# Kernel tuning notes

Measured on AMD Instinct MI355X. Metric: run time of the kernel, lower is better.

Reference implementation:

```python
import jax, jax.numpy as jnp
import numpy as np

N_NODES = 8192
SEQ = 256
H = 32  # lstm_hdim == gcn_hdim


def lstm_layer(x, Wih, Whh, bih, bhh, return_seq):
    # x: [B, S, D] -> torch nn.LSTM, gate order i,f,g,o
    B = x.shape[0]
    Hd = Whh.shape[1]
    b = bih + bhh

    def step(carry, xt):
        h, c = carry
        z = xt @ Wih.T + h @ Whh.T + b  # [B, 4H]
        i, f, g, o = jnp.split(z, 4, axis=-1)
        c = jax.nn.sigmoid(f) * c + jax.nn.sigmoid(i) * jnp.tanh(g)
        h = jax.nn.sigmoid(o) * jnp.tanh(c)
        return (h, c), (h if return_seq else None)

    init = (jnp.zeros((B, Hd), x.dtype), jnp.zeros((B, Hd), x.dtype))
    (h_n, _), ys = jax.lax.scan(step, init, jnp.transpose(x, (1, 0, 2)))
    if return_seq:
        ys = jnp.transpose(ys, (1, 0, 2))  # [B, S, H]
    return ys, h_n


def layer_norm(x, g, b, eps=1e-5):
    mu = jnp.mean(x, axis=-1, keepdims=True)
    var = jnp.mean((x - mu) ** 2, axis=-1, keepdims=True)
    return (x - mu) * jax.lax.rsqrt(var + eps) * g + b


def gcn_conv(x, edge_index, edge_weight, W, bias, n_nodes):
    # PyG GCNConv with self-loops (fill 1.0) and symmetric normalization.
    h = x @ W  # transform first (in_dim -> out_dim)
    src, dst = edge_index[0], edge_index[1]
    deg = jax.ops.segment_sum(edge_weight, dst, num_segments=n_nodes) + 1.0  # +1 self loop
    dinv = jnp.where(deg > 0, jax.lax.rsqrt(deg), 0.0)
    norm = dinv[src] * edge_weight * dinv[dst]  # [E]
    agg = jax.ops.segment_sum(norm[:, None] * h[src], dst, num_segments=n_nodes)
    agg = agg + h * (dinv * dinv)[:, None]  # self-loop message
    return agg + bias


def setup_inputs() -> dict:
    key = jax.random.key(0)
    ks = jax.random.split(key, 20)
    s = 0.1
    d = {
        "x": jax.random.normal(ks[0], (N_NODES, SEQ), jnp.float32),
        "edge_weight": jax.random.uniform(ks[1], (262144,), jnp.float32),
        "Wih1": jax.random.normal(ks[2], (4 * H, 1)) * s,
        "Whh1": jax.random.normal(ks[3], (4 * H, H)) * s,
        "bih1": jax.random.normal(ks[4], (4 * H,)) * s,
        "bhh1": jax.random.normal(ks[5], (4 * H,)) * s,
        "ln1_g": jnp.ones((H,), jnp.float32),
        "ln1_b": jnp.zeros((H,), jnp.float32),
        "Wih2": jax.random.normal(ks[6], (4 * H, H)) * s,
        "Whh2": jax.random.normal(ks[7], (4 * H, H)) * s,
        "bih2": jax.random.normal(ks[8], (4 * H,)) * s,
        "bhh2": jax.random.normal(ks[9], (4 * H,)) * s,
        "Wg1": jax.random.normal(ks[10], (H, H)) * s,
        "bg1": jax.random.normal(ks[11], (H,)) * s,
        "Wg2": jax.random.normal(ks[12], (H, H)) * s,
        "bg2": jax.random.normal(ks[13], (H,)) * s,
        "Wfc": jax.random.normal(ks[14], (2, H + 1)) * s,
        "bfc": jax.random.normal(ks[15], (2,)) * s,
        "edge_index": jax.random.randint(ks[16], (2, 262144), 0, N_NODES, jnp.int64 if jax.config.jax_enable_x64 else jnp.int32),
    }
    return d


def reference(x, edge_weight, Wih1, Whh1, bih1, bhh1, ln1_g, ln1_b,
              Wih2, Whh2, bih2, bhh2, Wg1, bg1, Wg2, bg2, Wfc, bfc, edge_index):
    n = x.shape[0]
    xs = x[:, :, None]  # [B, S, 1]
    # Temporal module (batched over all samples; dropout off in eval).
    y1, _ = lstm_layer(xs, Wih1, Whh1, bih1, bhh1, return_seq=True)
    y1 = layer_norm(y1, ln1_g, ln1_b)
    _, h2 = lstm_layer(y1, Wih2, Whh2, bih2, bhh2, return_seq=False)  # [B, H]
    gcn_in = h2  # lstm_out.view(-1, lstm_hdim)
    # Spatial module: 2 GCNConv + ELU (dropout between layers is identity in eval).
    g = jax.nn.elu(gcn_conv(gcn_in, edge_index, edge_weight, Wg1, bg1, n))
    g = jax.nn.elu(gcn_conv(g, edge_index, edge_weight, Wg2, bg2, n))
    feat = jnp.concatenate([gcn_in, jnp.mean(g, axis=1, keepdims=True)], axis=1)  # [B, H+1]
    out = feat @ Wfc.T + bfc
    return jax.nn.log_softmax(out, axis=1)
```

## Files before the change

kernel.cpp:

```cpp
#include <hip/hip_runtime.h>

typedef __attribute__((ext_vector_type(8))) short short8;
typedef __attribute__((ext_vector_type(4))) float float4v;

#define NNODES 8192
#define SEQLEN 256

static __device__ __forceinline__ float bf2f(unsigned short u) {
  union { unsigned u; float f; } v; v.u = ((unsigned)u) << 16; return v.f;
}
static __device__ __forceinline__ unsigned short f2bf(float f) {
  union { float f; unsigned u; } v; v.f = f;
  unsigned r = v.u + 0x7FFFu + ((v.u >> 16) & 1u);
  return (unsigned short)(r >> 16);
}
static __device__ __forceinline__ void splitbf8(const float* v, short8& hi) {
#pragma unroll
  for (int j = 0; j < 8; ++j) hi[j] = (short)f2bf(v[j]);
}

static __device__ __forceinline__ float lstm_cell(float zi, float zf, float zg,
                                                  float zo, float& c) {
  float ef = __builtin_amdgcn_exp2f(-zf);
  float ei = __builtin_amdgcn_exp2f(-zi);
  float eg = __builtin_amdgcn_exp2f(fminf(zg + zg, 60.f));
  float fterm = c * __builtin_amdgcn_rcpf(1.f + ef);
  float igt = (eg - 1.f) * __builtin_amdgcn_rcpf((1.f + ei) * (eg + 1.f));
  c = fterm + igt;
  float eo = __builtin_amdgcn_exp2f(-zo);
  float ec = __builtin_amdgcn_exp2f(fminf(2.88539008178f * c, 40.f));
  return (ec - 1.f) * __builtin_amdgcn_rcpf((1.f + eo) * (ec + 1.f));
}

__global__ __launch_bounds__(512, 4)
void lstm_fused(const float* __restrict__ x,
                const float* __restrict__ Wih1, const float* __restrict__ Whh1,
                const float* __restrict__ bih1, const float* __restrict__ bhh1,
                const float* __restrict__ ln_g, const float* __restrict__ ln_b,
                const float* __restrict__ Wih2, const float* __restrict__ Whh2,
                const float* __restrict__ bih2, const float* __restrict__ bhh2,
                const float* __restrict__ Wg1,
                float* __restrict__ h2out, float* __restrict__ hWa)
{
  const int tid = threadIdx.x;
  const int w = tid >> 6;
  const int lane = tid & 63;
  const int c = lane & 15;
  const int q = lane >> 4;
  const int cn = lane >> 2;
  const int ch = lane & 3;
  const int hid = w * 4 + ch;
  const int nodeBase = blockIdx.x * 16;
  const float L = 1.44269504089f;

  __shared__ __align__(16) float xlds[16 * 260];
  __shared__ __align__(16) float zbuf1[16 * 132];
  __shared__ __align__(16) float zbuf2[16 * 132];
  __shared__ __align__(16) unsigned short h1p[2][16 * 40];
  __shared__ __align__(16) unsigned short h2p[2][16 * 40];
  __shared__ __align__(16) float mu2[32];
  __shared__ __align__(16) float wgbuf[32 * 33];
  __shared__ __align__(16) float h2f[16 * 33];

  for (int i = tid; i < 16 * 256; i += 512) {
    int nn = i >> 8, tt = i & 255;
    xlds[nn * 260 + tt] = x[(size_t)(nodeBase + nn) * SEQLEN + tt];
  }
  if (tid < 64) xlds[(tid >> 2) * 260 + 256 + (tid & 3)] = 0.f;
  for (int i = tid; i < 1024; i += 512) wgbuf[(i >> 5) * 33 + (i & 31)] = Wg1[i];

  const int brow = (c & 3) * 32 + w * 4 + (c >> 2);
  short8 Bh1, Bi2, Bh2;
  float Gpre, b1pre, b2pre;
  {
    float v[8];
#pragma unroll
    for (int j = 0; j < 8; ++j) v[j] = L * Whh1[brow * 32 + q * 8 + j];
    splitbf8(v, Bh1);
#pragma unroll
    for (int j = 0; j < 8; ++j) v[j] = L * Wih2[brow * 32 + q * 8 + j] * ln_g[q * 8 + j];
    splitbf8(v, Bi2);
#pragma unroll
    for (int j = 0; j < 8; ++j) v[j] = L * Whh2[brow * 32 + q * 8 + j];
    splitbf8(v, Bh2);
    float sG = 0.f, sB = 0.f;
    for (int k = 0; k < 32; ++k) {
      sG += Wih2[brow * 32 + k] * ln_g[k];
      sB += Wih2[brow * 32 + k] * ln_b[k];
    }
    Gpre = L * sG;
    b1pre = L * (bih1[brow] + bhh1[brow]);
    b2pre = L * (sB + bih2[brow] + bhh2[brow]);
  }
  const float4v C1 = {b1pre, b1pre, b1pre, b1pre};
  const float4v C2 = {b2pre, b2pre, b2pre, b2pre};
  const float4v z4 = {0.f, 0.f, 0.f, 0.f};
  float w1v[4];
#pragma unroll
  for (int g = 0; g < 4; ++g) w1v[g] = L * Wih1[g * 32 + hid];

  int zW[4];
#pragma unroll
  for (int r = 0; r < 4; ++r) zW[r] = (q * 4 + r) * 132 + w * 16 + c;
  const int zR = cn * 132 + hid * 4;
  const int hWr = cn * 40 + hid;
  const int hRd = c * 40 + q * 8;

  short8 h1A = {0,0,0,0,0,0,0,0};
  short8 h2A = {0,0,0,0,0,0,0,0};
  float c1 = 0.f, c2 = 0.f, hv2 = 0.f;
  __syncthreads();

  {
    float4v za = __builtin_amdgcn_mfma_f32_16x16x32_bf16(h1A, Bh1, C1, 0, 0, 0);
#pragma unroll
    for (int r = 0; r < 4; ++r) zbuf1[zW[r]] = za[r];
    float4v zv = *(const float4v*)&zbuf1[zR];
    float xv = xlds[cn * 260 + 0];
    float hv = lstm_cell(fmaf(xv, w1v[0], zv[0]), fmaf(xv, w1v[1], zv[1]),
                         fmaf(xv, w1v[2], zv[2]), fmaf(xv, w1v[3], zv[3]), c1);
    h1p[1][hWr] = f2bf(hv);
  }
  __syncthreads();
  h1A = *(const short8*)&h1p[1][hRd];

  for (int t = 0; t < SEQLEN; ++t) {
    const int pl = t & 1;
    float4v za = __builtin_amdgcn_mfma_f32_16x16x32_bf16(h1A, Bh1, C1, 0, 0, 0);
    float4v db = __builtin_amdgcn_mfma_f32_16x16x32_bf16(h2A, Bh2, C2, 0, 0, 0);

    float s = 0.f, s2 = 0.f;
#pragma unroll
    for (int j = 0; j < 8; ++j) {
      float hf = bf2f((unsigned short)h1A[j]);
      s += hf; s2 = fmaf(hf, hf, s2);
    }
    s  += __shfl_xor(s, 16, 64);  s  += __shfl_xor(s, 32, 64);
    s2 += __shfl_xor(s2, 16, 64); s2 += __shfl_xor(s2, 32, 64);
    float mu = s * (1.f / 32.f);
    float var = s2 * (1.f / 32.f) - mu * mu;
    float rstd = rsqrtf(var + 1e-5f);
    if (q < 2) mu2[c * 2 + q] = (q == 0) ? rstd : rstd * mu;

    float4v da = __builtin_amdgcn_mfma_f32_16x16x32_bf16(h1A, Bi2, z4, 0, 0, 0);
#pragma unroll
    for (int r = 0; r < 4; ++r) {
      float2 ab = *(const float2*)&mu2[(q * 4 + r) * 2];
      zbuf2[zW[r]] = fmaf(ab.x, da[r], fmaf(-ab.y, Gpre, db[r]));
      zbuf1[zW[r]] = za[r];
    }
    {
      float4v zv = *(const float4v*)&zbuf2[zR];
      hv2 = lstm_cell(zv[0], zv[1], zv[2], zv[3], c2);
      h2p[pl][hWr] = f2bf(hv2);
    }
    {
      float4v zv = *(const float4v*)&zbuf1[zR];
      float xv = xlds[cn * 260 + t + 1];
      float hv = lstm_cell(fmaf(xv, w1v[0], zv[0]), fmaf(xv, w1v[1], zv[1]),
                           fmaf(xv, w1v[2], zv[2]), fmaf(xv, w1v[3], zv[3]), c1);
      h1p[pl][hWr] = f2bf(hv);
    }
    __syncthreads();
    h1A = *(const short8*)&h1p[pl][hRd];
    h2A = *(const short8*)&h2p[pl][hRd];
  }

  h2out[(size_t)(nodeBase + cn) * 32 + hid] = hv2;

  __syncthreads();
  h2f[cn * 33 + hid] = hv2;
  __syncthreads();
  {
    int nl = tid >> 5, j = tid & 31;
    float acc = 0.f;
#pragma unroll
    for (int k = 0; k < 32; ++k) acc = fmaf(h2f[nl * 33 + k], wgbuf[k * 33 + j], acc);
    hWa[(size_t)(nodeBase + nl) * 32 + j] = acc;
  }
}

__global__ void count_k(const int* __restrict__ ei, const float* __restrict__ ew,
                        unsigned long long* __restrict__ pk, int E) {
  int e = blockIdx.x * 256 + threadIdx.x;
  if (e >= E) return;
  int d = ei[E + e];
  unsigned long long pay = (1ull << 40) |
      (unsigned long long)(unsigned)(ew[e] * 16777216.f + 0.5f);
  atomicAdd(&pk[d], pay);
}

__global__ __launch_bounds__(1024, 1)
void scan_k(const unsigned long long* __restrict__ pk, int* __restrict__ off,
            int* __restrict__ pos, float* __restrict__ dinv) {
  __shared__ int wtot[16];
  __shared__ int wexcl[16];
  int tid = threadIdx.x;
  int wv = tid >> 6, lane = tid & 63;
  int base = tid * 8;
  int v[8]; int sum = 0;
#pragma unroll
  for (int i = 0; i < 8; ++i) {
    unsigned long long u = pk[base + i];
    v[i] = (int)(u >> 40);
    float degv = (float)(u & 0xFFFFFFFFFFull) * (1.f / 16777216.f);
    dinv[base + i] = rsqrtf(degv + 1.0f);
    sum += v[i];
  }
  int incl = sum;
#pragma unroll
  for (int d = 1; d < 64; d <<= 1) {
    int t = __shfl_up(incl, d, 64);
    if (lane >= d) incl += t;
  }
  if (lane == 63) wtot[wv] = incl;
  __syncthreads();
  if (wv == 0 && lane < 16) {
    int wval = wtot[lane];
    int wincl = wval;
#pragma unroll
    for (int d = 1; d < 16; d <<= 1) {
      int t = __shfl_up(wincl, d, 64);
      if (lane >= d) wincl += t;
    }
    wexcl[lane] = wincl - wval;
  }
  __syncthreads();
  int run = wexcl[wv] + (incl - sum);
#pragma unroll
  for (int i = 0; i < 8; ++i) {
    off[base + i] = run; pos[base + i] = run; run += v[i];
  }
  if (tid == 1023) off[8192] = run;
}

__global__ void scatter_k(const int* __restrict__ ei, const float* __restrict__ ew,
                          const float* __restrict__ dinv, int* __restrict__ pos,
                          int2* __restrict__ ed, int E) {
  int e = blockIdx.x * 256 + threadIdx.x;
  if (e >= E) return;
  int sidx = ei[e], d = ei[E + e];
  int p = atomicAdd(&pos[d], 1);
  int2 pay;
  pay.x = sidx;
  pay.y = __float_as_int(dinv[sidx] * ew[e] * dinv[d]);
  ed[p] = pay;
}

__global__ __launch_bounds__(512, 4)
void gather_mid_k(const int* __restrict__ off, const int2* __restrict__ ed,
                  const float* __restrict__ dinv, const float* __restrict__ hWa,
                  const float* __restrict__ bg1, const float* __restrict__ Wg2,
                  float* __restrict__ aggB) {
  __shared__ float wg[32 * 33];
  __shared__ float g1buf[16][33];
  int tid = threadIdx.x;
  for (int i = tid; i < 1024; i += 512) wg[(i >> 5) * 33 + (i & 31)] = Wg2[i];
  int nl = tid >> 5, j = tid & 31;
  int node = blockIdx.x * 16 + nl;
  float dv = dinv[node];
  float a0 = dv * dv * hWa[(size_t)node * 32 + j];
  float a1 = 0.f, a2 = 0.f, a3 = 0.f;
  int p0 = off[node], p1 = off[node + 1];
  int p = p0;
  for (; p + 3 < p1; p += 4) {
    int2 e0 = ed[p], e1 = ed[p + 1], e2 = ed[p + 2], e3 = ed[p + 3];
    a0 = fmaf(__int_as_float(e0.y), hWa[(size_t)e0.x * 32 + j], a0);
    a1 = fmaf(__int_as_float(e1.y), hWa[(size_t)e1.x * 32 + j], a1);
    a2 = fmaf(__int_as_float(e2.y), hWa[(size_t)e2.x * 32 + j], a2);
    a3 = fmaf(__int_as_float(e3.y), hWa[(size_t)e3.x * 32 + j], a3);
  }
  for (; p < p1; ++p) {
    int2 e0 = ed[p];
    a0 = fmaf(__int_as_float(e0.y), hWa[(size_t)e0.x * 32 + j], a0);
  }
  float v = (a0 + a1) + (a2 + a3) + bg1[j];
  g1buf[nl][j] = (v > 0.f) ? v : expm1f(v);
  __syncthreads();
  float acc = 0.f;
#pragma unroll
  for (int k = 0; k < 32; ++k) acc = fmaf(g1buf[nl][k], wg[k * 33 + j], acc);
  aggB[(size_t)node * 32 + j] = acc;
}

__global__ __launch_bounds__(512, 4)
void gather_final_k(const int* __restrict__ off, const int2* __restrict__ ed,
                    const float* __restrict__ dinv, const float* __restrict__ aggB,
                    const float* __restrict__ bg2, const float* __restrict__ h2o,
                    const float* __restrict__ Wfc, const float* __restrict__ bfc,
                    float* __restrict__ out) {
  int tid = threadIdx.x;
  int nl = tid >> 5, j = tid & 31;
  int node = blockIdx.x * 16 + nl;
  float dv = dinv[node];
  float a0 = dv * dv * aggB[(size_t)node * 32 + j];
  float a1 = 0.f, a2 = 0.f, a3 = 0.f;
  int p0 = off[node], p1 = off[node + 1];
  int p = p0;
  for (; p + 3 < p1; p += 4) {
    int2 e0 = ed[p], e1 = ed[p + 1], e2 = ed[p + 2], e3 = ed[p + 3];
    a0 = fmaf(__int_as_float(e0.y), aggB[(size_t)e0.x * 32 + j], a0);
    a1 = fmaf(__int_as_float(e1.y), aggB[(size_t)e1.x * 32 + j], a1);
    a2 = fmaf(__int_as_float(e2.y), aggB[(size_t)e2.x * 32 + j], a2);
    a3 = fmaf(__int_as_float(e3.y), aggB[(size_t)e3.x * 32 + j], a3);
  }
  for (; p < p1; ++p) {
    int2 e0 = ed[p];
    a0 = fmaf(__int_as_float(e0.y), aggB[(size_t)e0.x * 32 + j], a0);
  }
  float v = (a0 + a1) + (a2 + a3) + bg2[j];
  float e = (v > 0.f) ? v : expm1f(v);
  float h2v = h2o[(size_t)node * 32 + j];
  float p0s = h2v * Wfc[j];
  float p1s = h2v * Wfc[33 + j];
#pragma unroll
  for (int m = 1; m < 32; m <<= 1) {
    e   += __shfl_xor(e, m, 32);
    p0s += __shfl_xor(p0s, m, 32);
    p1s += __shfl_xor(p1s, m, 32);
  }
  if (j == 0) {
    float mean = e * (1.f / 32.f);
    float o0 = p0s + mean * Wfc[32] + bfc[0];
    float o1 = p1s + mean * Wfc[65] + bfc[1];
    float mx = fmaxf(o0, o1);
    float l = mx + logf(expf(o0 - mx) + expf(o1 - mx));
    out[node * 2 + 0] = o0 - l;
    out[node * 2 + 1] = o1 - l;
  }
}

extern "C" void kernel_launch(void* const* d_in, const int* in_sizes, int n_in,
                              void* d_out, int out_size, void* d_ws, size_t ws_size,
                              hipStream_t stream) {
  const float* x    = (const float*)d_in[0];
  const float* ew   = (const float*)d_in[1];
  const float* Wih1 = (const float*)d_in[2];
  const float* Whh1 = (const float*)d_in[3];
  const float* bih1 = (const float*)d_in[4];
  const float* bhh1 = (const float*)d_in[5];
  const float* ln_g = (const float*)d_in[6];
  const float* ln_b = (const float*)d_in[7];
  const float* Wih2 = (const float*)d_in[8];
  const float* Whh2 = (const float*)d_in[9];
  const float* bih2 = (const float*)d_in[10];
  const float* bhh2 = (const float*)d_in[11];
  const float* Wg1  = (const float*)d_in[12];
  const float* bg1  = (const float*)d_in[13];
  const float* Wg2  = (const float*)d_in[14];
  const float* bg2  = (const float*)d_in[15];
  const float* Wfc  = (const float*)d_in[16];
  const float* bfc  = (const float*)d_in[17];
  const int* ei     = (const int*)d_in[18];
  float* out = (float*)d_out;
  const int E = in_sizes[1];

  float* ws   = (float*)d_ws;
  float* h2o  = ws;
  float* hWa  = ws + 262144;
  float* aggB = ws + 524288;
  unsigned long long* pk = (unsigned long long*)(ws + 786432);
  float* dinv = ws + 802816;
  int*   off  = (int*)(ws + 811008);
  int*   pos  = (int*)(ws + 819208);
  int2*  ed   = (int2*)(ws + 827400);

  hipMemsetAsync((void*)pk, 0, 8192 * sizeof(unsigned long long), stream);
  hipLaunchKernelGGL(count_k, dim3((E + 255) / 256), dim3(256), 0, stream, ei, ew, pk, E);
  hipLaunchKernelGGL(lstm_fused, dim3(NNODES / 16), dim3(512), 0, stream,
                     x, Wih1, Whh1, bih1, bhh1, ln_g, ln_b,
                     Wih2, Whh2, bih2, bhh2, Wg1, h2o, hWa);
  hipLaunchKernelGGL(scan_k, dim3(1), dim3(1024), 0, stream, pk, off, pos, dinv);
  hipLaunchKernelGGL(scatter_k, dim3((E + 255) / 256), dim3(256), 0, stream, ei, ew, dinv, pos, ed, E);
  hipLaunchKernelGGL(gather_mid_k, dim3(NNODES / 16), dim3(512), 0, stream,
                     off, ed, dinv, hWa, bg1, Wg2, aggB);
  hipLaunchKernelGGL(gather_final_k, dim3(NNODES / 16), dim3(512), 0, stream,
                     off, ed, dinv, aggB, bg2, h2o, Wfc, bfc, out);
}
```

Baseline: 438.3 us.

## Swap MFMA operands so gate outputs land per-lane, removing LDS transposes

Swaps the A/B operands of the recurrent MFMAs so each lane directly receives the four gates (i,f,g,o) for its own hidden unit and node. This removes the per-step zbuf1/zbuf2 LDS write-then-read transposes and the mu2 LDS exchange of LayerNorm statistics, which are now available in-lane. Biases and the LayerNorm correction term become per-row vectors in the accumulator. The serial 256-step recurrence loses several LDS round trips per step, at the cost of a re-mapped thread-to-hidden-unit layout that has to stay consistent with the h buffers.

```diff
diff --git a/kernel.cpp b/kernel.cpp
--- a/kernel.cpp
+++ b/kernel.cpp
@@ -47,18 +47,13 @@
   const int lane = tid & 63;
   const int c = lane & 15;
   const int q = lane >> 4;
-  const int cn = lane >> 2;
-  const int ch = lane & 3;
-  const int hid = w * 4 + ch;
+  const int hid = w * 4 + q;
   const int nodeBase = blockIdx.x * 16;
   const float L = 1.44269504089f;
 
   __shared__ __align__(16) float xlds[16 * 260];
-  __shared__ __align__(16) float zbuf1[16 * 132];
-  __shared__ __align__(16) float zbuf2[16 * 132];
   __shared__ __align__(16) unsigned short h1p[2][16 * 40];
   __shared__ __align__(16) unsigned short h2p[2][16 * 40];
-  __shared__ __align__(16) float mu2[32];
   __shared__ __align__(16) float wgbuf[32 * 33];
   __shared__ __align__(16) float h2f[16 * 33];
 
@@ -69,41 +64,43 @@
   if (tid < 64) xlds[(tid >> 2) * 260 + 256 + (tid & 3)] = 0.f;
   for (int i = tid; i < 1024; i += 512) wgbuf[(i >> 5) * 33 + (i & 31)] = Wg1[i];
 
-  const int brow = (c & 3) * 32 + w * 4 + (c >> 2);
+  const int browF = (c & 3) * 32 + w * 4 + (c >> 2);
   short8 Bh1, Bi2, Bh2;
-  float Gpre, b1pre, b2pre;
   {
     float v[8];
 #pragma unroll
-    for (int j = 0; j < 8; ++j) v[j] = L * Whh1[brow * 32 + q * 8 + j];
+    for (int j = 0; j < 8; ++j) v[j] = L * Whh1[browF * 32 + q * 8 + j];
     splitbf8(v, Bh1);
 #pragma unroll
-    for (int j = 0; j < 8; ++j) v[j] = L * Wih2[brow * 32 + q * 8 + j] * ln_g[q * 8 + j];
+    for (int j = 0; j < 8; ++j) v[j] = L * Wih2[browF * 32 + q * 8 + j] * ln_g[q * 8 + j];
     splitbf8(v, Bi2);
 #pragma unroll
-    for (int j = 0; j < 8; ++j) v[j] = L * Whh2[brow * 32 + q * 8 + j];
+    for (int j = 0; j < 8; ++j) v[j] = L * Whh2[browF * 32 + q * 8 + j];
     splitbf8(v, Bh2);
+  }
+
+  float Gp[4], C1a[4], C2a[4];
+#pragma unroll
+  for (int r = 0; r < 4; ++r) {
+    const int br = r * 32 + hid;
     float sG = 0.f, sB = 0.f;
     for (int k = 0; k < 32; ++k) {
-      sG += Wih2[brow * 32 + k] * ln_g[k];
-      sB += Wih2[brow * 32 + k] * ln_b[k];
-    }
-    Gpre = L * sG;
-    b1pre = L * (bih1[brow] + bhh1[brow]);
-    b2pre = L * (sB + bih2[brow] + bhh2[brow]);
-  }
-  const float4v C1 = {b1pre, b1pre, b1pre, b1pre};
-  const float4v C2 = {b2pre, b2pre, b2pre, b2pre};
+      float wv = Wih2[br * 32 + k];
+      sG += wv * ln_g[k];
+      sB += wv * ln_b[k];
+    }
+    Gp[r] = L * sG;
+    C1a[r] = L * (bih1[br] + bhh1[br]);
+    C2a[r] = L * (sB + bih2[br] + bhh2[br]);
+  }
+  const float4v C1 = {C1a[0], C1a[1], C1a[2], C1a[3]};
+  const float4v C2 = {C2a[0], C2a[1], C2a[2], C2a[3]};
   const float4v z4 = {0.f, 0.f, 0.f, 0.f};
   float w1v[4];
 #pragma unroll
   for (int g = 0; g < 4; ++g) w1v[g] = L * Wih1[g * 32 + hid];
 
-  int zW[4];
-#pragma unroll
-  for (int r = 0; r < 4; ++r) zW[r] = (q * 4 + r) * 132 + w * 16 + c;
-  const int zR = cn * 132 + hid * 4;
-  const int hWr = cn * 40 + hid;
+  const int hWr = c * 40 + hid;
   const int hRd = c * 40 + q * 8;
 
   short8 h1A = {0,0,0,0,0,0,0,0};
@@ -112,13 +109,9 @@
   __syncthreads();
 
   {
-    float4v za = __builtin_amdgcn_mfma_f32_16x16x32_bf16(h1A, Bh1, C1, 0, 0, 0);
-#pragma unroll
-    for (int r = 0; r < 4; ++r) zbuf1[zW[r]] = za[r];
-    float4v zv = *(const float4v*)&zbuf1[zR];
-    float xv = xlds[cn * 260 + 0];
-    float hv = lstm_cell(fmaf(xv, w1v[0], zv[0]), fmaf(xv, w1v[1], zv[1]),
-                         fmaf(xv, w1v[2], zv[2]), fmaf(xv, w1v[3], zv[3]), c1);
+    float xv = xlds[c * 260 + 0];
+    float hv = lstm_cell(fmaf(xv, w1v[0], C1[0]), fmaf(xv, w1v[1], C1[1]),
+                         fmaf(xv, w1v[2], C1[2]), fmaf(xv, w1v[3], C1[3]), c1);
     h1p[1][hWr] = f2bf(hv);
   }
   __syncthreads();
@@ -126,8 +119,8 @@
 
   for (int t = 0; t < SEQLEN; ++t) {
     const int pl = t & 1;
-    float4v za = __builtin_amdgcn_mfma_f32_16x16x32_bf16(h1A, Bh1, C1, 0, 0, 0);
-    float4v db = __builtin_amdgcn_mfma_f32_16x16x32_bf16(h2A, Bh2, C2, 0, 0, 0);
+    float4v za = __builtin_amdgcn_mfma_f32_16x16x32_bf16(Bh1, h1A, C1, 0, 0, 0);
+    float4v db = __builtin_amdgcn_mfma_f32_16x16x32_bf16(Bh2, h2A, C2, 0, 0, 0);
 
     float s = 0.f, s2 = 0.f;
 #pragma unroll
@@ -140,25 +133,22 @@
     float mu = s * (1.f / 32.f);
     float var = s2 * (1.f / 32.f) - mu * mu;
     float rstd = rsqrtf(var + 1e-5f);
-    if (q < 2) mu2[c * 2 + q] = (q == 0) ? rstd : rstd * mu;
-
-    float4v da = __builtin_amdgcn_mfma_f32_16x16x32_bf16(h1A, Bi2, z4, 0, 0, 0);
-#pragma unroll
-    for (int r = 0; r < 4; ++r) {
-      float2 ab = *(const float2*)&mu2[(q * 4 + r) * 2];
-      zbuf2[zW[r]] = fmaf(ab.x, da[r], fmaf(-ab.y, Gpre, db[r]));
-      zbuf1[zW[r]] = za[r];
-    }
+    float mur = rstd * mu;
+
+    float4v da = __builtin_amdgcn_mfma_f32_16x16x32_bf16(Bi2, h1A, z4, 0, 0, 0);
+
     {
-      float4v zv = *(const float4v*)&zbuf2[zR];
-      hv2 = lstm_cell(zv[0], zv[1], zv[2], zv[3], c2);
+      float z20 = fmaf(rstd, da[0], fmaf(-mur, Gp[0], db[0]));
+      float z21 = fmaf(rstd, da[1], fmaf(-mur, Gp[1], db[1]));
+      float z22 = fmaf(rstd, da[2], fmaf(-mur, Gp[2], db[2]));
+      float z23 = fmaf(rstd, da[3], fmaf(-mur, Gp[3], db[3]));
+      hv2 = lstm_cell(z20, z21, z22, z23, c2);
       h2p[pl][hWr] = f2bf(hv2);
     }
     {
-      float4v zv = *(const float4v*)&zbuf1[zR];
-      float xv = xlds[cn * 260 + t + 1];
-      float hv = lstm_cell(fmaf(xv, w1v[0], zv[0]), fmaf(xv, w1v[1], zv[1]),
-                           fmaf(xv, w1v[2], zv[2]), fmaf(xv, w1v[3], zv[3]), c1);
+      float xv = xlds[c * 260 + t + 1];
+      float hv = lstm_cell(fmaf(xv, w1v[0], za[0]), fmaf(xv, w1v[1], za[1]),
+                           fmaf(xv, w1v[2], za[2]), fmaf(xv, w1v[3], za[3]), c1);
       h1p[pl][hWr] = f2bf(hv);
     }
     __syncthreads();
@@ -166,10 +156,9 @@
     h2A = *(const short8*)&h2p[pl][hRd];
   }
 
-  h2out[(size_t)(nodeBase + cn) * 32 + hid] = hv2;
-
-  __syncthreads();
-  h2f[cn * 33 + hid] = hv2;
+  h2out[(size_t)(nodeBase + c) * 32 + hid] = hv2;
+
+  h2f[c * 33 + hid] = hv2;
   __syncthreads();
   {
     int nl = tid >> 5, j = tid & 31;
```

Result: faster. 392.9 us (-10.3%).
